# Kernel optimization log

Measured on AMD Instinct MI355X. Metric: run time of the kernel, lower is better.

Reference implementation:

```python
import jax, jax.numpy as jnp
import numpy as np

N = 20000; E = 320000; G = 64; IN = 64; HID = 128; H = 8; HD = H * HID  # 1024


def setup_inputs() -> dict:
    key = jax.random.key(0)
    ks = jax.random.split(key, 32)
    inp = {}
    inp['x'] = jax.random.normal(ks[0], (N, IN), jnp.float32)
    inp['edge_index'] = jax.random.randint(ks[1], (2, E), 0, N, dtype=jnp.int64)
    inp['batch'] = jnp.sort(jax.random.randint(ks[2], (N,), 0, G, dtype=jnp.int64))
    dims_in = [IN, HD, HD]
    k = 3
    for i in range(3):
        d_in = dims_in[i]
        inp[f'gat_W{i}'] = jax.random.normal(ks[k], (d_in, HD), jnp.float32) * (1.0 / np.sqrt(d_in)); k += 1
        inp[f'gat_b{i}'] = jnp.zeros((HD,), jnp.float32)
        inp[f'att_src{i}'] = jax.random.normal(ks[k], (H, HID), jnp.float32) * 0.1; k += 1
        inp[f'att_dst{i}'] = jax.random.normal(ks[k], (H, HID), jnp.float32) * 0.1; k += 1
    for i in range(2):
        inp[f'boot_W{i}'] = jax.random.normal(ks[k], (HD, HD), jnp.float32) * (1.0 / np.sqrt(HD)); k += 1
        inp[f'boot_b{i}'] = jnp.zeros((HD,), jnp.float32)
    inp['clf_W1'] = jax.random.normal(ks[k], (HD, HID), jnp.float32) * (1.0 / np.sqrt(HD)); k += 1
    inp['clf_b1'] = jnp.zeros((HID,), jnp.float32)
    inp['clf_W2'] = jax.random.normal(ks[k], (HID, 2), jnp.float32) * (1.0 / np.sqrt(HID)); k += 1
    inp['clf_b2'] = jnp.zeros((2,), jnp.float32)
    return inp


def _gat_layer(x, W, b, a_src, a_dst, src, dst):
    # PyG GATConv (concat=True, self-loops already appended, eval mode => no dropout)
    h = (x @ W).reshape(N, H, HID)                      # [N,H,D]
    s = jnp.einsum('nhd,hd->nh', h, a_src)              # [N,H]
    t = jnp.einsum('nhd,hd->nh', h, a_dst)              # [N,H]
    e = jax.nn.leaky_relu(s[src] + t[dst], 0.2)         # [Etot,H]
    m = jax.ops.segment_max(e, dst, num_segments=N)     # segment softmax over incoming edges
    m = jnp.where(jnp.isfinite(m), m, 0.0)
    ex = jnp.exp(e - m[dst])
    denom = jax.ops.segment_sum(ex, dst, num_segments=N)
    alpha = ex / jnp.maximum(denom[dst], 1e-16)         # [Etot,H]
    out = jax.ops.segment_sum(alpha[:, :, None] * h[src], dst, num_segments=N)  # [N,H,D]
    return out.reshape(N, HD) + b


def reference(x, edge_index, batch,
              gat_W0, gat_b0, att_src0, att_dst0,
              gat_W1, gat_b1, att_src1, att_dst1,
              gat_W2, gat_b2, att_src2, att_dst2,
              boot_W0, boot_b0, boot_W1, boot_b1,
              clf_W1, clf_b1, clf_W2, clf_b2):
    loop = jnp.arange(N, dtype=edge_index.dtype)
    src = jnp.concatenate([edge_index[0], loop])
    dst = jnp.concatenate([edge_index[1], loop])
    gat = [(gat_W0, gat_b0, att_src0, att_dst0),
           (gat_W1, gat_b1, att_src1, att_dst1),
           (gat_W2, gat_b2, att_src2, att_dst2)]
    boot = [(boot_W0, boot_b0), (boot_W1, boot_b1)]
    h = x
    for i in range(3):
        W, b, a_s, a_d = gat[i]
        h = jax.nn.elu(_gat_layer(h, W, b, a_s, a_d, src, dst))
        if i < 2:
            noise = jax.random.normal(jax.random.key(100 + i), h.shape, h.dtype) * 0.1
            bW, bb = boot[i]
            h = (h + noise) @ bW + bb
    # global mean pool over graphs
    sums = jax.ops.segment_sum(h, batch, num_segments=G)        # [G,HD]
    cnts = jax.ops.segment_sum(jnp.ones((N,), h.dtype), batch, num_segments=G)
    g = sums / jnp.maximum(cnts, 1.0)[:, None]
    z = jax.nn.relu(g @ clf_W1 + clf_b1)                        # dropout = identity (eval)
    return z @ clf_W2 + clf_b2
```

## Files before the change

### kernel.cpp

```cpp
#include <hip/hip_runtime.h>
#include <stdint.h>

#define N_NODES 20000
#define N_EDGES 320000
#define E_TOT   (N_EDGES + N_NODES)
#define NGRAPH  64
#define DIN     64
#define DHID    128
#define NHEAD   8
#define HDIM    1024

typedef unsigned int u32;
typedef unsigned short u16;
typedef __bf16 bfx8 __attribute__((ext_vector_type(8)));
typedef float f32x4 __attribute__((ext_vector_type(4)));
typedef float f32x2 __attribute__((ext_vector_type(2)));

__device__ __forceinline__ u16 f2bf(float f){
  u32 u = __float_as_uint(f);
  u32 r = (u + 0x7FFFu + ((u >> 16) & 1u)) >> 16;
  return (u16)r;
}
__device__ __forceinline__ float bf2f(u16 v){
  return __uint_as_float(((u32)v) << 16);
}
__device__ __forceinline__ f32x2 up2(u32 u){
  f32x2 v;
  v.x = __uint_as_float(u << 16);
  v.y = __uint_as_float(u & 0xffff0000u);
  return v;
}

typedef __attribute__((address_space(3))) u32 lds_u32_t;
typedef const __attribute__((address_space(1))) u32 glb_u32_t;
__device__ __forceinline__ void g2l16(const void* g, void* l){
  __builtin_amdgcn_global_load_lds((glb_u32_t*)(uintptr_t)g,
                                   (lds_u32_t*)(uintptr_t)l, 16, 0, 0);
}

__device__ __forceinline__ u32 rotl32(u32 x, int r){ return (x<<r) | (x>>(32-r)); }

__device__ __forceinline__ void threefry2x32(u32 k0, u32 k1, u32 x0, u32 x1,
                                             u32& y0, u32& y1){
  u32 k2 = k0 ^ k1 ^ 0x1BD11BDAu;
  x0 += k0; x1 += k1;
#define TFR(r) { x0 += x1; x1 = rotl32(x1, (r)); x1 ^= x0; }
  TFR(13) TFR(15) TFR(26) TFR(6)
  x0 += k1; x1 += k2 + 1u;
  TFR(17) TFR(29) TFR(16) TFR(24)
  x0 += k2; x1 += k0 + 2u;
  TFR(13) TFR(15) TFR(26) TFR(6)
  x0 += k0; x1 += k1 + 3u;
  TFR(17) TFR(29) TFR(16) TFR(24)
  x0 += k1; x1 += k2 + 4u;
  TFR(13) TFR(15) TFR(26) TFR(6)
  x0 += k2; x1 += k0 + 5u;
#undef TFR
  y0 = x0; y1 = x1;
}

__device__ __forceinline__ float erfinv_fast(float x){
  float t = fmaf(-x, x, 1.0f);
  float w = -__logf(t);
  float p;
  if (w < 5.0f){
    w -= 2.5f;
    p = 2.81022636e-08f;
    p = fmaf(p, w, 3.43273939e-07f);
    p = fmaf(p, w, -3.5233877e-06f);
    p = fmaf(p, w, -4.39150654e-06f);
    p = fmaf(p, w, 0.00021858087f);
    p = fmaf(p, w, -0.00125372503f);
    p = fmaf(p, w, -0.00417768164f);
    p = fmaf(p, w, 0.246640727f);
    p = fmaf(p, w, 1.50140941f);
  } else {
    w = sqrtf(w) - 3.0f;
    p = -0.000200214257f;
    p = fmaf(p, w, 0.000100950558f);
    p = fmaf(p, w, 0.00134934322f);
    p = fmaf(p, w, -0.00367342844f);
    p = fmaf(p, w, 0.00573950773f);
    p = fmaf(p, w, -0.0076224613f);
    p = fmaf(p, w, 0.00943887047f);
    p = fmaf(p, w, 1.00167406f);
    p = fmaf(p, w, 2.83297682f);
  }
  return p * x;
}

__device__ __forceinline__ float jax_normal(u32 seed, u32 i){
  u32 y0, y1;
  threefry2x32(0u, seed, 0u, i, y0, y1);
  u32 bits = y0 ^ y1;
  float f = __uint_as_float((bits >> 9) | 0x3f800000u) - 1.0f;
  float xx = fmaxf(-0.99999994f, fmaf(f, 2.0f, -0.99999994f));
  return 1.41421356f * erfinv_fast(xx);
}

__global__ __launch_bounds__(256) void prep_misc_kernel(const float* __restrict__ x,
    const float* __restrict__ W0, const float* __restrict__ W1,
    u16* __restrict__ xbf, u16* __restrict__ O0, u16* __restrict__ O1,
    const int* __restrict__ ei, const int* __restrict__ batch,
    int* __restrict__ cnt, int* __restrict__ gcnt,
    const float* __restrict__ gatW0, const float* __restrict__ asrc0,
    const float* __restrict__ adst0, float* __restrict__ wst){
  const int z = blockIdx.y;
  if (z < 3){
    const float* S = (z==0) ? W0 : (z==1) ? W1 : x;
    u16* D = (z==0) ? O0 : (z==1) ? O1 : xbf;
    const int total = (z==2) ? N_NODES*DIN : HDIM*HDIM;
    int i = (blockIdx.x*256 + threadIdx.x)*4;
    if (i < total){
      float4 v = *(const float4*)(S + i);
      D[i+0] = f2bf(v.x); D[i+1] = f2bf(v.y);
      D[i+2] = f2bf(v.z); D[i+3] = f2bf(v.w);
    }
  } else if (z == 3){
    int i = blockIdx.x*256 + threadIdx.x;
    if (i < N_EDGES) atomicAdd(&cnt[ei[N_EDGES + i]], 1);
    else if (i < E_TOT) atomicAdd(&gcnt[batch[i - N_EDGES]], 1);
  } else {
    if (blockIdx.x == 0){
      for (int o = threadIdx.x; o < DIN*16; o += 256){
        const int d = o >> 4, c = o & 15;
        const int hh = c & 7;
        const float* av = ((c < 8) ? asrc0 : adst0) + hh*DHID;
        const float* wr = gatW0 + (size_t)d*HDIM + hh*DHID;
        float a = 0.f;
        for (int k = 0; k < DHID; ++k) a = fmaf(wr[k], av[k], a);
        wst[o] = a;
      }
    }
  }
}

__global__ __launch_bounds__(256) void st0_kernel(const float* __restrict__ x,
    const float* __restrict__ wst, float* __restrict__ sbuf,
    float* __restrict__ tbuf){
  const int n = blockIdx.x*256 + threadIdx.x;
  if (n >= N_NODES) return;
  float acc[16];
#pragma unroll
  for (int c = 0; c < 16; ++c) acc[c] = 0.f;
  const float* xr = x + (size_t)n*DIN;
  for (int d = 0; d < DIN; d += 4){
    const float4 xv = *(const float4*)(xr + d);
    const float* w0 = wst + d*16;
#pragma unroll
    for (int c = 0; c < 16; ++c){
      acc[c] = fmaf(xv.x, w0[c],      acc[c]);
      acc[c] = fmaf(xv.y, w0[16+c],   acc[c]);
      acc[c] = fmaf(xv.z, w0[32+c],   acc[c]);
      acc[c] = fmaf(xv.w, w0[48+c],   acc[c]);
    }
  }
#pragma unroll
  for (int h = 0; h < NHEAD; ++h){
    sbuf[n*NHEAD + h] = acc[h];
    tbuf[n*NHEAD + h] = acc[8 + h];
  }
}

__global__ __launch_bounds__(256) void transpose_all_kernel(
    const float* __restrict__ W0, const float* __restrict__ W1,
    const float* __restrict__ W2,
    u16* __restrict__ T0, u16* __restrict__ T1, u16* __restrict__ T2){
  const int z = blockIdx.z;
  const float* W = (z==0)?W0:(z==1)?W1:W2;
  u16* T = (z==0)?T0:(z==1)?T1:T2;
  const int K = (z==0)?DIN:HDIM;
  const int bk = blockIdx.y*32;
  if (bk >= K) return;
  __shared__ float t[32][33];
  int bn = blockIdx.x*32;
  int lx = threadIdx.x & 31, ly = threadIdx.x >> 5;
#pragma unroll
  for (int r = 0; r < 32; r += 8)
    t[ly+r][lx] = W[(size_t)(bk+ly+r)*HDIM + bn + lx];
  __syncthreads();
#pragma unroll
  for (int r = 0; r < 32; r += 8){
    const u16 v = f2bf(t[lx][ly+r]);
    if (z == 0){
      const size_t base = (size_t)(bn+ly+r)*128 + bk + lx;
      T[base] = v; T[base + 64] = v;
    } else {
      T[(size_t)(bn+ly+r)*K + bk + lx] = v;
    }
  }
}

__global__ __launch_bounds__(1024) void scan_pair_kernel(const int* __restrict__ cnt,
    int* __restrict__ rowptr, int* __restrict__ cursor, int* __restrict__ colidx,
    const int* __restrict__ gcnt, int* __restrict__ goff){
  if (blockIdx.x == 1){
    if (threadIdx.x == 0){
      int s = 0;
      for (int g = 0; g < NGRAPH; ++g){ goff[g] = s; s += gcnt[g]; }
      goff[NGRAPH] = s;
    }
    return;
  }
  __shared__ int wsum[16];
  __shared__ int carry_s;
  const int tid = threadIdx.x, lane = tid & 63, wv = tid >> 6;
  if (tid == 0){ carry_s = 0; rowptr[0] = 0; }
  __syncthreads();
  for (int base = 0; base < N_NODES; base += 1024){
    int i = base + tid;
    int v = (i < N_NODES) ? cnt[i] + 1 : 0;
    int s = v;
#pragma unroll
    for (int off = 1; off < 64; off <<= 1){
      int t = __shfl_up(s, off);
      if (lane >= off) s += t;
    }
    if (lane == 63) wsum[wv] = s;
    __syncthreads();
    if (wv == 0 && lane < 16){
      int ws = wsum[lane];
#pragma unroll
      for (int off = 1; off < 16; off <<= 1){
        int t = __shfl_up(ws, off);
        if (lane >= off) ws += t;
      }
      wsum[lane] = ws;
    }
    __syncthreads();
    int incl = s + ((wv > 0) ? wsum[wv-1] : 0) + carry_s;
    if (i < N_NODES){
      rowptr[i+1] = incl;
      const int slot = incl - v;
      colidx[slot] = i;
      cursor[i] = slot + 1;
    }
    __syncthreads();
    if (tid == 1023) carry_s = incl;
    __syncthreads();
  }
}

__global__ __launch_bounds__(256) void fill_edges_kernel(const int* __restrict__ ei,
    int* __restrict__ cursor, int* __restrict__ colidx){
  int e = blockIdx.x*256 + threadIdx.x;
  if (e < N_EDGES){
    int s = ei[e], d = ei[N_EDGES + e];
    int p = atomicAdd(&cursor[d], 1);
    colidx[p] = s;
  }
}

__device__ __forceinline__ void gemm_tile(const u16* __restrict__ A,
    const u16* __restrict__ BT, const float* __restrict__ bias,
    u16* __restrict__ Cb, int M, int K, int bm, int bn,
    u16* As, u16* Bs,
    const float* __restrict__ asrc, const float* __restrict__ adst,
    float* __restrict__ sbuf, float* __restrict__ tbuf,
    const int emode, const u32 seed){
  const int tid = threadIdx.x;
  const int lane = tid & 63, w = tid >> 6;
  const int wm = (w & 1)*64, wn = (w >> 1)*64;

  const int cid0 = tid, cid1 = 256 + tid;
  const int r0 = cid0 & 127, kc0 = cid0 >> 7;
  const int r1 = cid1 & 127, kc1 = cid1 >> 7;
  int ar0 = bm + r0; if (ar0 >= M) ar0 = M - 1;
  int ar1 = bm + r1; if (ar1 >= M) ar1 = M - 1;
  const u16* ag0 = A + (size_t)ar0*K + kc0*8;
  const u16* ag1 = A + (size_t)ar1*K + kc1*8;
  const u16* bg0 = BT + (size_t)(bn + r0)*K + kc0*8;
  const u16* bg1 = BT + (size_t)(bn + r1)*K + kc1*8;
  u16* al0 = As + cid0*8;  u16* al1 = As + cid1*8;
  u16* bl0 = Bs + cid0*8;  u16* bl1 = Bs + cid1*8;

  const int rowl = lane & 15, kg = lane >> 4;
  const bfx8* ap = (const bfx8*)(As + ((size_t)kg*128 + wm + rowl)*8);
  const bfx8* bp = (const bfx8*)(Bs + ((size_t)kg*128 + wn + rowl)*8);

  f32x4 acc[4][4] = {};
  for (int k0 = 0; k0 < K; k0 += 32){
    g2l16(ag0 + k0, al0);
    g2l16(ag1 + k0, al1);
    g2l16(bg0 + k0, bl0);
    g2l16(bg1 + k0, bl1);
    __syncthreads();
    bfx8 af[4], bfr[4];
#pragma unroll
    for (int i = 0; i < 4; ++i){ af[i] = ap[i*16]; bfr[i] = bp[i*16]; }
#pragma unroll
    for (int i = 0; i < 4; ++i)
#pragma unroll
      for (int j = 0; j < 4; ++j)
        acc[j][i] = __builtin_amdgcn_mfma_f32_16x16x32_bf16(bfr[j], af[i], acc[j][i], 0, 0, 0);
    __syncthreads();
  }

  const int quad = lane >> 4;
  const bool dost = (sbuf != nullptr);
  const int head = bn >> 7;
  float sl[4] = {0.f,0.f,0.f,0.f}, tl[4] = {0.f,0.f,0.f,0.f};
#pragma unroll
  for (int j = 0; j < 4; ++j){
    const int col0 = bn + wn + j*16 + quad*4;
    float4 bv = make_float4(0.f,0.f,0.f,0.f);
    if (bias) bv = *(const float4*)(bias + col0);
    float4 av = make_float4(0.f,0.f,0.f,0.f), dv = av;
    if (dost){
      const int d0 = col0 - bn;
      av = *(const float4*)(asrc + head*DHID + d0);
      dv = *(const float4*)(adst + head*DHID + d0);
    }
#pragma unroll
    for (int i = 0; i < 4; ++i){
      const int row = bm + wm + i*16 + rowl;
      if (emode == 1){
        if (row < M){
          float v0 = acc[j][i][0] + bv.x;
          float v1 = acc[j][i][1] + bv.y;
          float v2 = acc[j][i][2] + bv.z;
          float v3 = acc[j][i][3] + bv.w;
          v0 = (v0 > 0.f) ? v0 : __expf(v0) - 1.0f;
          v1 = (v1 > 0.f) ? v1 : __expf(v1) - 1.0f;
          v2 = (v2 > 0.f) ? v2 : __expf(v2) - 1.0f;
          v3 = (v3 > 0.f) ? v3 : __expf(v3) - 1.0f;
          const u32 ib = (u32)row*HDIM + (u32)col0;
          v0 = fmaf(0.1f, jax_normal(seed, ib+0u), v0);
          v1 = fmaf(0.1f, jax_normal(seed, ib+1u), v1);
          v2 = fmaf(0.1f, jax_normal(seed, ib+2u), v2);
          v3 = fmaf(0.1f, jax_normal(seed, ib+3u), v3);
          uint2 pk;
          pk.x = (u32)f2bf(v0) | ((u32)f2bf(v1) << 16);
          pk.y = (u32)f2bf(v2) | ((u32)f2bf(v3) << 16);
          *(uint2*)(Cb + (size_t)row*HDIM + col0) = pk;
        }
      } else {
        const u16 p0 = f2bf(acc[j][i][0] + bv.x);
        const u16 p1 = f2bf(acc[j][i][1] + bv.y);
        const u16 p2 = f2bf(acc[j][i][2] + bv.z);
        const u16 p3 = f2bf(acc[j][i][3] + bv.w);
        if (row < M){
          uint2 pk;
          pk.x = (u32)p0 | ((u32)p1 << 16);
          pk.y = (u32)p2 | ((u32)p3 << 16);
          *(uint2*)(Cb + (size_t)row*HDIM + col0) = pk;
        }
        if (dost){
          const float c0 = bf2f(p0), c1 = bf2f(p1), c2 = bf2f(p2), c3 = bf2f(p3);
          sl[i] = fmaf(c0, av.x, fmaf(c1, av.y, fmaf(c2, av.z, fmaf(c3, av.w, sl[i]))));
          tl[i] = fmaf(c0, dv.x, fmaf(c1, dv.y, fmaf(c2, dv.z, fmaf(c3, dv.w, tl[i]))));
        }
      }
    }
  }
  if (dost){
#pragma unroll
    for (int i = 0; i < 4; ++i){
      sl[i] += __shfl_xor(sl[i], 16); sl[i] += __shfl_xor(sl[i], 32);
      tl[i] += __shfl_xor(tl[i], 16); tl[i] += __shfl_xor(tl[i], 32);
    }
    float* sred = (float*)As;
    float* tred = sred + 128;
    if ((w >> 1) == 0 && quad == 0){
#pragma unroll
      for (int i = 0; i < 4; ++i){
        const int rl = wm + i*16 + rowl;
        sred[rl] = sl[i]; tred[rl] = tl[i];
      }
    }
    __syncthreads();
    if ((w >> 1) == 1 && quad == 0){
#pragma unroll
      for (int i = 0; i < 4; ++i){
        const int rl = wm + i*16 + rowl;
        const int row = bm + rl;
        if (row < M){
          sbuf[row*NHEAD + head] = sred[rl] + sl[i];
          tbuf[row*NHEAD + head] = tred[rl] + tl[i];
        }
      }
    }
  }
}

__global__ __launch_bounds__(256) void gemm_bf16(
    const u16* __restrict__ A, const u16* __restrict__ BT,
    const float* __restrict__ bias, u16* __restrict__ Cb, int M, int K,
    const float* __restrict__ asrc, const float* __restrict__ adst,
    float* __restrict__ sbuf, float* __restrict__ tbuf){
  __shared__ __align__(16) u16 As[4*128*8];
  __shared__ __align__(16) u16 Bs[4*128*8];
  const int kblk = blockIdx.y*8 + blockIdx.x;
  const int xc = kblk & 7, bq = (kblk >> 3) & 7, gq = kblk >> 6;
  const int bmi = gq*8 + xc;
  const int mt = (M + 127) >> 7;
  if (bmi >= mt) return;
  gemm_tile(A, BT, bias, Cb, M, K, bmi*128, bq*128, As, Bs,
            asrc, adst, sbuf, tbuf, 0, 0u);
}

__global__ __launch_bounds__(256) void gemm_l0t(
    const u16* __restrict__ agg2, const u16* __restrict__ BT,
    const float* __restrict__ bias, u16* __restrict__ Cb, u32 seed){
  __shared__ __align__(16) u16 As[4*128*8];
  __shared__ __align__(16) u16 Bs[4*128*8];
  const int head = blockIdx.x;
  const int bm = blockIdx.y*128;
  gemm_tile(agg2 + (size_t)head*N_NODES*128, BT, bias, Cb, N_NODES, 128,
            bm, head*128, As, Bs, nullptr, nullptr, nullptr, nullptr,
            1, seed);
}

__global__ __launch_bounds__(256) void wf_bias_kernel(
    const u16* __restrict__ A0, const u16* __restrict__ B0, u16* __restrict__ C0,
    const u16* __restrict__ A1, const u16* __restrict__ B1, u16* __restrict__ C1,
    const float* __restrict__ bb0, const u16* __restrict__ gwt0,
    const float* __restrict__ bb1, const u16* __restrict__ gwt1,
    float* __restrict__ fb0, float* __restrict__ fb1){
  __shared__ __align__(16) u16 As[4*128*8];
  __shared__ __align__(16) u16 Bs[4*128*8];
  if (blockIdx.z < 2){
    const u16* A = blockIdx.z ? A1 : A0;
    const u16* B = blockIdx.z ? B1 : B0;
    u16* C = blockIdx.z ? C1 : C0;
    gemm_tile(A, B, nullptr, C, HDIM, HDIM, blockIdx.y*128, blockIdx.x*128,
              As, Bs, nullptr, nullptr, nullptr, nullptr, 0, 0u);
  } else {
    const int kb = blockIdx.y*8 + blockIdx.x;
    const int wv = threadIdx.x >> 6, lane = threadIdx.x & 63;
    for (int idx = kb*4 + wv; idx < 2*HDIM; idx += 256){
      const int set = idx >> 10, n = idx & (HDIM-1);
      const float* bb = set ? bb1 : bb0;
      const u16* row = (set ? gwt1 : gwt0) + (size_t)n*HDIM + lane*16;
      const float* bp = bb + lane*16;
      float acc = 0.f;
#pragma unroll
      for (int k = 0; k < 16; ++k) acc = fmaf(bp[k], bf2f(row[k]), acc);
      for (int off = 32; off > 0; off >>= 1) acc += __shfl_down(acc, off);
      if (lane == 0) (set ? fb1 : fb0)[n] = acc;
    }
  }
}

__device__ __forceinline__ void gat_core(const u16* __restrict__ hlin,
    const float* __restrict__ sbuf, const float* __restrict__ tbuf,
    const int* __restrict__ rowptr, const int* __restrict__ colidx,
    const float* __restrict__ bias, const int n, const int lane,
    float o[16]){
  const int jsub = lane >> 3;
  const int hh   = lane & 7;
  const int hA   = lane >> 3;
  const int row0 = rowptr[n];
  const int deg  = rowptr[n+1] - row0;
  const float tn = tbuf[n*NHEAD + hh];
  const char* hl = (const char*)hlin;
  const u32 lb   = (u32)lane << 5;

  f32x2 acc[8] = {};
  float m_run = -INFINITY, d_run = 0.f;

  for (int c = 0; c < deg; c += 8){
    const int ne = min(8, deg - c);
    const int jj = (jsub < ne) ? jsub : (ne - 1);
    const int srcv = colidx[row0 + c + jj];
    float e = sbuf[srcv*NHEAD + hh] + tn;
    e = (e > 0.f) ? e : 0.2f*e;
    if (jsub >= ne) e = -INFINITY;
    float mc = e;
    mc = fmaxf(mc, __shfl_xor(mc, 8));
    mc = fmaxf(mc, __shfl_xor(mc, 16));
    mc = fmaxf(mc, __shfl_xor(mc, 32));
    const float mnew = fmaxf(m_run, mc);
    const float w = __expf(e - mnew);
    float ws = w;
    ws += __shfl_xor(ws, 8);
    ws += __shfl_xor(ws, 16);
    ws += __shfl_xor(ws, 32);
    const float r = (m_run == -INFINITY) ? 0.0f : __expf(m_run - mnew);
    d_run = fmaf(d_run, r, ws);
    m_run = mnew;
    const float rA = __shfl(r, hA);
    const f32x2 r2 = {rA, rA};
#pragma unroll
    for (int q = 0; q < 8; ++q) acc[q] *= r2;
    int j = 0;
    for (; j + 2 <= ne; j += 2){
      const int s0 = __builtin_amdgcn_readlane(srcv, j*8);
      const int s1 = __builtin_amdgcn_readlane(srcv, j*8 + 8);
      const float w0 = __shfl(w, j*8 + hA);
      const float w1 = __shfl(w, j*8 + 8 + hA);
      const char* rp0 = hl + (((size_t)(u32)s0) << 11);
      const char* rp1 = hl + (((size_t)(u32)s1) << 11);
      const uint4 a0 = *(const uint4*)(rp0 + lb);
      const uint4 a1 = *(const uint4*)(rp0 + lb + 16);
      const uint4 b0 = *(const uint4*)(rp1 + lb);
      const uint4 b1 = *(const uint4*)(rp1 + lb + 16);
      const f32x2 w02 = {w0, w0}, w12 = {w1, w1};
      acc[0] = __builtin_elementwise_fma(w02, up2(a0.x), acc[0]);
      acc[1] = __builtin_elementwise_fma(w02, up2(a0.y), acc[1]);
      acc[2] = __builtin_elementwise_fma(w02, up2(a0.z), acc[2]);
      acc[3] = __builtin_elementwise_fma(w02, up2(a0.w), acc[3]);
      acc[4] = __builtin_elementwise_fma(w02, up2(a1.x), acc[4]);
      acc[5] = __builtin_elementwise_fma(w02, up2(a1.y), acc[5]);
      acc[6] = __builtin_elementwise_fma(w02, up2(a1.z), acc[6]);
      acc[7] = __builtin_elementwise_fma(w02, up2(a1.w), acc[7]);
      acc[0] = __builtin_elementwise_fma(w12, up2(b0.x), acc[0]);
      acc[1] = __builtin_elementwise_fma(w12, up2(b0.y), acc[1]);
      acc[2] = __builtin_elementwise_fma(w12, up2(b0.z), acc[2]);
      acc[3] = __builtin_elementwise_fma(w12, up2(b0.w), acc[3]);
      acc[4] = __builtin_elementwise_fma(w12, up2(b1.x), acc[4]);
      acc[5] = __builtin_elementwise_fma(w12, up2(b1.y), acc[5]);
      acc[6] = __builtin_elementwise_fma(w12, up2(b1.z), acc[6]);
      acc[7] = __builtin_elementwise_fma(w12, up2(b1.w), acc[7]);
    }
    if (j < ne){
      const int s0 = __builtin_amdgcn_readlane(srcv, j*8);
      const float w0 = __shfl(w, j*8 + hA);
      const char* rp0 = hl + (((size_t)(u32)s0) << 11);
      const uint4 a0 = *(const uint4*)(rp0 + lb);
      const uint4 a1 = *(const uint4*)(rp0 + lb + 16);
      const f32x2 w02 = {w0, w0};
      acc[0] = __builtin_elementwise_fma(w02, up2(a0.x), acc[0]);
      acc[1] = __builtin_elementwise_fma(w02, up2(a0.y), acc[1]);
      acc[2] = __builtin_elementwise_fma(w02, up2(a0.z), acc[2]);
      acc[3] = __builtin_elementwise_fma(w02, up2(a0.w), acc[3]);
      acc[4] = __builtin_elementwise_fma(w02, up2(a1.x), acc[4]);
      acc[5] = __builtin_elementwise_fma(w02, up2(a1.y), acc[5]);
      acc[6] = __builtin_elementwise_fma(w02, up2(a1.z), acc[6]);
      acc[7] = __builtin_elementwise_fma(w02, up2(a1.w), acc[7]);
    }
  }

  const float dA = __shfl(d_run, hA);
  const float invA = 1.0f / fmaxf(dA, 1e-16f);
#pragma unroll
  for (int q = 0; q < 8; ++q){ o[2*q] = acc[q].x; o[2*q+1] = acc[q].y; }
  const float4* bp = (const float4*)(bias + lane*16);
#pragma unroll
  for (int q = 0; q < 4; ++q){
    const float4 bv = bp[q];
    o[4*q+0] = fmaf(o[4*q+0], invA, bv.x);
    o[4*q+1] = fmaf(o[4*q+1], invA, bv.y);
    o[4*q+2] = fmaf(o[4*q+2], invA, bv.z);
    o[4*q+3] = fmaf(o[4*q+3], invA, bv.w);
  }
#pragma unroll
  for (int k = 0; k < 16; ++k)
    o[k] = (o[k] > 0.f) ? o[k] : __expf(o[k]) - 1.0f;
}

__global__ __launch_bounds__(256) void gat_agg_noise_kernel(
    const u16* __restrict__ hlin,
    const float* __restrict__ sbuf, const float* __restrict__ tbuf,
    const int* __restrict__ rowptr, const int* __restrict__ colidx,
    const float* __restrict__ bias, u16* __restrict__ outbf, u32 seed){
  const int tid  = threadIdx.x;
  const int lane = tid & 63;
  const int n    = blockIdx.x*4 + (tid >> 6);
  float o[16];
  gat_core(hlin, sbuf, tbuf, rowptr, colidx, bias, n, lane, o);
  const u32 ib = (u32)n*HDIM + (u32)lane*16u;
  u32 pk[8];
#pragma unroll
  for (int q = 0; q < 8; ++q){
    const float v0 = fmaf(0.1f, jax_normal(seed, ib + 2u*q + 0u), o[2*q+0]);
    const float v1 = fmaf(0.1f, jax_normal(seed, ib + 2u*q + 1u), o[2*q+1]);
    pk[q] = (u32)f2bf(v0) | ((u32)f2bf(v1) << 16);
  }
  uint4* dst = (uint4*)(outbf + (size_t)n*HDIM + lane*16);
  dst[0] = make_uint4(pk[0], pk[1], pk[2], pk[3]);
  dst[1] = make_uint4(pk[4], pk[5], pk[6], pk[7]);
}

__global__ __launch_bounds__(256) void gat_agg_pool_kernel(
    const u16* __restrict__ hlin,
    const float* __restrict__ sbuf, const float* __restrict__ tbuf,
    const int* __restrict__ rowptr, const int* __restrict__ colidx,
    const float* __restrict__ bias,
    const int* __restrict__ batch, float* __restrict__ gsum8){
  __shared__ float red[4][HDIM];
  const int tid  = threadIdx.x;
  const int lane = tid & 63;
  const int wv   = tid >> 6;
  const int n    = blockIdx.x*4 + wv;
  float o[16];
  gat_core(hlin, sbuf, tbuf, rowptr, colidx, bias, n, lane, o);
  float* rw = &red[wv][lane*16];
#pragma unroll
  for (int q = 0; q < 4; ++q)
    *(float4*)(rw + q*4) = make_float4(o[4*q], o[4*q+1], o[4*q+2], o[4*q+3]);
  __syncthreads();
  const int rep = blockIdx.x & 7;
  const int g0 = batch[blockIdx.x*4];
  const int g3 = batch[blockIdx.x*4 + 3];
  if (g0 == g3){
    const int d = tid*4;
    float4 s;
    s.x = red[0][d+0] + red[1][d+0] + red[2][d+0] + red[3][d+0];
    s.y = red[0][d+1] + red[1][d+1] + red[2][d+1] + red[3][d+1];
    s.z = red[0][d+2] + red[1][d+2] + red[2][d+2] + red[3][d+2];
    s.w = red[0][d+3] + red[1][d+3] + red[2][d+3] + red[3][d+3];
    float* gp = gsum8 + ((size_t)rep*NGRAPH + g0)*HDIM + d;
    atomicAdd(gp+0, s.x); atomicAdd(gp+1, s.y);
    atomicAdd(gp+2, s.z); atomicAdd(gp+3, s.w);
  } else {
    const int gn = batch[n];
    float* gp = gsum8 + ((size_t)rep*NGRAPH + gn)*HDIM + lane*16;
#pragma unroll
    for (int k = 0; k < 16; ++k) atomicAdd(gp + k, o[k]);
  }
}

__global__ __launch_bounds__(256) void agg_x_kernel(const u16* __restrict__ xbf,
    const float* __restrict__ sbuf, const float* __restrict__ tbuf,
    const int* __restrict__ rowptr, const int* __restrict__ colidx,
    u16* __restrict__ agg2){
  const int tid  = threadIdx.x;
  const int lane = tid & 63;
  const int n    = blockIdx.x*4 + (tid >> 6);
  const int jsub = lane >> 3;
  const int hh   = lane & 7;
  const int hA   = lane >> 3;
  const int row0 = rowptr[n];
  const int deg  = rowptr[n+1] - row0;
  const float tn = tbuf[n*NHEAD + hh];
  const char* xb = (const char*)xbf;
  const u32 lb   = (u32)(lane & 7) << 4;

  f32x2 acc[4] = {};
  float m_run = -INFINITY, d_run = 0.f;

  for (int c = 0; c < deg; c += 8){
    const int ne = min(8, deg - c);
    const int jj = (jsub < ne) ? jsub : (ne - 1);
    const int srcv = colidx[row0 + c + jj];
    float e = sbuf[srcv*NHEAD + hh] + tn;
    e = (e > 0.f) ? e : 0.2f*e;
    if (jsub >= ne) e = -INFINITY;
    float mc = e;
    mc = fmaxf(mc, __shfl_xor(mc, 8));
    mc = fmaxf(mc, __shfl_xor(mc, 16));
    mc = fmaxf(mc, __shfl_xor(mc, 32));
    const float mnew = fmaxf(m_run, mc);
    const float w = __expf(e - mnew);
    float ws = w;
    ws += __shfl_xor(ws, 8);
    ws += __shfl_xor(ws, 16);
    ws += __shfl_xor(ws, 32);
    const float r = (m_run == -INFINITY) ? 0.0f : __expf(m_run - mnew);
    d_run = fmaf(d_run, r, ws);
    m_run = mnew;
    const float rA = __shfl(r, hA);
    const f32x2 r2 = {rA, rA};
#pragma unroll
    for (int q = 0; q < 4; ++q) acc[q] *= r2;
    int j = 0;
    for (; j + 2 <= ne; j += 2){
      const int s0 = __builtin_amdgcn_readlane(srcv, j*8);
      const int s1 = __builtin_amdgcn_readlane(srcv, j*8 + 8);
      const float w0 = __shfl(w, j*8 + hA);
      const float w1 = __shfl(w, j*8 + 8 + hA);
      const uint4 a0 = *(const uint4*)(xb + (((size_t)(u32)s0) << 7) + lb);
      const uint4 b0 = *(const uint4*)(xb + (((size_t)(u32)s1) << 7) + lb);
      const f32x2 w02 = {w0, w0}, w12 = {w1, w1};
      acc[0] = __builtin_elementwise_fma(w02, up2(a0.x), acc[0]);
      acc[1] = __builtin_elementwise_fma(w02, up2(a0.y), acc[1]);
      acc[2] = __builtin_elementwise_fma(w02, up2(a0.z), acc[2]);
      acc[3] = __builtin_elementwise_fma(w02, up2(a0.w), acc[3]);
      acc[0] = __builtin_elementwise_fma(w12, up2(b0.x), acc[0]);
      acc[1] = __builtin_elementwise_fma(w12, up2(b0.y), acc[1]);
      acc[2] = __builtin_elementwise_fma(w12, up2(b0.z), acc[2]);
      acc[3] = __builtin_elementwise_fma(w12, up2(b0.w), acc[3]);
    }
    if (j < ne){
      const int s0 = __builtin_amdgcn_readlane(srcv, j*8);
      const float w0 = __shfl(w, j*8 + hA);
      const uint4 a0 = *(const uint4*)(xb + (((size_t)(u32)s0) << 7) + lb);
      const f32x2 w02 = {w0, w0};
      acc[0] = __builtin_elementwise_fma(w02, up2(a0.x), acc[0]);
      acc[1] = __builtin_elementwise_fma(w02, up2(a0.y), acc[1]);
      acc[2] = __builtin_elementwise_fma(w02, up2(a0.z), acc[2]);
      acc[3] = __builtin_elementwise_fma(w02, up2(a0.w), acc[3]);
    }
  }

  const float dA = __shfl(d_run, hA);
  const float invA = 1.0f / fmaxf(dA, 1e-16f);
  float v[8];
#pragma unroll
  for (int q = 0; q < 4; ++q){ v[2*q] = acc[q].x*invA; v[2*q+1] = acc[q].y*invA; }
  u32 hp[4], lp[4];
#pragma unroll
  for (int q = 0; q < 4; ++q){
    const u16 h0 = f2bf(v[2*q]),   h1 = f2bf(v[2*q+1]);
    const u16 l0 = f2bf(v[2*q]   - bf2f(h0));
    const u16 l1 = f2bf(v[2*q+1] - bf2f(h1));
    hp[q] = (u32)h0 | ((u32)h1 << 16);
    lp[q] = (u32)l0 | ((u32)l1 << 16);
  }
  u16* base = agg2 + ((size_t)hA*N_NODES + (size_t)n)*128 + (lane & 7)*8;
  *(uint4*)(base)      = make_uint4(hp[0], hp[1], hp[2], hp[3]);
  *(uint4*)(base + 64) = make_uint4(lp[0], lp[1], lp[2], lp[3]);
}

__global__ __launch_bounds__(256) void pool_clf_kernel(const float* __restrict__ gsum8,
    const int* __restrict__ gcnt,
    const float* __restrict__ W1, const float* __restrict__ b1,
    const float* __restrict__ W2, const float* __restrict__ b2,
    float* __restrict__ out){
  __shared__ float gs[HDIM];
  __shared__ float z[DHID];
  const int g = blockIdx.x, tid = threadIdx.x;
  const int cb = tid*4;
  const float invc = 1.0f / fmaxf((float)gcnt[g], 1.0f);
  float4 s = make_float4(0.f,0.f,0.f,0.f);
#pragma unroll
  for (int r = 0; r < 8; ++r){
    const float4 v = *(const float4*)(gsum8 + ((size_t)r*NGRAPH + g)*HDIM + cb);
    s.x += v.x; s.y += v.y; s.z += v.z; s.w += v.w;
  }
  gs[cb+0] = s.x*invc; gs[cb+1] = s.y*invc;
  gs[cb+2] = s.z*invc; gs[cb+3] = s.w*invc;
  __syncthreads();
  if (tid < DHID){
    float a = b1[tid];
    for (int k = 0; k < HDIM; ++k) a = fmaf(gs[k], W1[k*DHID + tid], a);
    z[tid] = fmaxf(a, 0.0f);
  }
  __syncthreads();
  if (tid < 2){
    float o = b2[tid];
    for (int k = 0; k < DHID; ++k) o = fmaf(z[k], W2[k*2 + tid], o);
    out[g*2 + tid] = o;
  }
}

extern "C" void kernel_launch(void* const* d_in, const int* in_sizes, int n_in,
                              void* d_out, int out_size, void* d_ws, size_t ws_size,
                              hipStream_t stream){
  const float* x      = (const float*)d_in[0];
  const int*   ei     = (const int*)d_in[1];
  const int*   batch  = (const int*)d_in[2];
  const float* gatW[3]  = {(const float*)d_in[3],  (const float*)d_in[7],  (const float*)d_in[11]};
  const float* gatB[3]  = {(const float*)d_in[4],  (const float*)d_in[8],  (const float*)d_in[12]};
  const float* asrc[3]  = {(const float*)d_in[5],  (const float*)d_in[9],  (const float*)d_in[13]};
  const float* adst[3]  = {(const float*)d_in[6],  (const float*)d_in[10], (const float*)d_in[14]};
  const float* bootW[2] = {(const float*)d_in[15], (const float*)d_in[17]};
  const float* bootB[2] = {(const float*)d_in[16], (const float*)d_in[18]};
  const float* clfW1 = (const float*)d_in[19];
  const float* clfb1 = (const float*)d_in[20];
  const float* clfW2 = (const float*)d_in[21];
  const float* clfb2 = (const float*)d_in[22];
  float* outp = (float*)d_out;

  float* fws  = (float*)d_ws;
  float* hB   = fws;
  float* sbuf = hB + (size_t)N_NODES*HDIM;
  float* tbuf = sbuf + (size_t)N_NODES*NHEAD;
  float* fbias0 = tbuf + (size_t)N_NODES*NHEAD;
  float* fbias1 = fbias0 + HDIM;
  u16* xbf    = (u16*)(fbias1 + HDIM);
  u16* hAbf   = xbf + (size_t)N_NODES*DIN;
  u16* hBbf   = hAbf + (size_t)N_NODES*HDIM;
  u16* wt[3];
  wt[0] = hBbf + (size_t)N_NODES*HDIM;
  wt[1] = wt[0] + (size_t)HDIM*128;
  wt[2] = wt[1] + (size_t)HDIM*HDIM;
  u16* wnt0   = wt[2] + (size_t)HDIM*HDIM;
  u16* wnt1   = wnt0 + (size_t)HDIM*HDIM;
  u16* wf0    = wnt1 + (size_t)HDIM*HDIM;
  u16* wf1    = wf0 + (size_t)HDIM*HDIM;
  int* rowptr = (int*)(wf1 + (size_t)HDIM*HDIM);
  int* cursor = rowptr + (N_NODES+1);
  int* colidx = cursor + N_NODES;
  int* gcnt   = colidx + E_TOT;
  int* cnt    = gcnt + NGRAPH;
  float* gsum8 = (float*)(cnt + N_NODES);
  int* goff   = (int*)(gsum8 + (size_t)8*NGRAPH*HDIM);
  float* wst  = (float*)(goff + NGRAPH + 1);

  u16* agg2 = hAbf;

  (void)hipMemsetAsync(gcnt, 0,
      (NGRAPH + N_NODES + (size_t)8*NGRAPH*HDIM)*sizeof(int), stream);

  const int nb_e = (N_EDGES + 255)/256;

  prep_misc_kernel<<<dim3((E_TOT + 255)/256, 5), 256, 0, stream>>>(
      x, bootW[0], bootW[1], xbf, wnt0, wnt1, ei, batch, cnt, gcnt,
      gatW[0], asrc[0], adst[0], wst);
  st0_kernel<<<(N_NODES + 255)/256, 256, 0, stream>>>(x, wst, sbuf, tbuf);
  transpose_all_kernel<<<dim3(HDIM/32, HDIM/32, 3), 256, 0, stream>>>(
      gatW[0], gatW[1], gatW[2], wt[0], wt[1], wt[2]);
  scan_pair_kernel<<<2, 1024, 0, stream>>>(cnt, rowptr, cursor, colidx, gcnt, goff);
  fill_edges_kernel<<<nb_e, 256, 0, stream>>>(ei, cursor, colidx);

  wf_bias_kernel<<<dim3(8, 8, 3), 256, 0, stream>>>(
      wt[1], wnt0, wf0, wt[2], wnt1, wf1,
      bootB[0], wt[1], bootB[1], wt[2], fbias0, fbias1);

  const int mt = (N_NODES + 127)/128;
  dim3 gemmGrid(8, (mt + 7)/8*8);

  agg_x_kernel<<<N_NODES/4, 256, 0, stream>>>(xbf, sbuf, tbuf, rowptr, colidx,
                                              agg2);
  gemm_l0t<<<dim3(8, mt), 256, 0, stream>>>(agg2, wt[0], gatB[0], hBbf, 100u);

  gemm_bf16<<<gemmGrid, 256, 0, stream>>>(hBbf, wf0, fbias0, hAbf, N_NODES, HDIM,
                                          asrc[1], adst[1], sbuf, tbuf);
  gat_agg_noise_kernel<<<N_NODES/4, 256, 0, stream>>>(hAbf, sbuf, tbuf, rowptr,
                                                      colidx, gatB[1], hBbf, 101u);
  gemm_bf16<<<gemmGrid, 256, 0, stream>>>(hBbf, wf1, fbias1, hAbf, N_NODES, HDIM,
                                          asrc[2], adst[2], sbuf, tbuf);
  gat_agg_pool_kernel<<<N_NODES/4, 256, 0, stream>>>(hAbf, sbuf, tbuf, rowptr,
                                                     colidx, gatB[2], batch, gsum8);

  pool_clf_kernel<<<NGRAPH, 256, 0, stream>>>(gsum8, gcnt,
                                              clfW1, clfb1, clfW2, clfb2, outp);
}
```

Baseline: 829.7 us.

## Unroll edge gather loop by three and replace pooling atomics with partial-sum reduction

The edge aggregation loops in gat_core and agg_x now process three neighbour rows per iteration instead of two, with two- and one-edge tails. This puts more independent gathers in flight per wave. The final-layer pooling no longer does float atomics into eight replicated per-graph buffers. Blocks whose four nodes share a graph write their partial sums to a per-block scratch array, and a new pool_reduce_kernel sums those per graph; atomics remain only for boundary blocks. This adds a kernel launch and extra scratch traffic, and the unroll raises register pressure.

```diff
diff --git a/kernel.cpp b/kernel.cpp
--- a/kernel.cpp
+++ b/kernel.cpp
@@ -442,6 +442,16 @@
   }
 }
 
+#define EDGE_FMA(WV, R0, R1)                                              \
+  acc[0] = __builtin_elementwise_fma(WV, up2(R0.x), acc[0]);              \
+  acc[1] = __builtin_elementwise_fma(WV, up2(R0.y), acc[1]);              \
+  acc[2] = __builtin_elementwise_fma(WV, up2(R0.z), acc[2]);              \
+  acc[3] = __builtin_elementwise_fma(WV, up2(R0.w), acc[3]);              \
+  acc[4] = __builtin_elementwise_fma(WV, up2(R1.x), acc[4]);              \
+  acc[5] = __builtin_elementwise_fma(WV, up2(R1.y), acc[5]);              \
+  acc[6] = __builtin_elementwise_fma(WV, up2(R1.z), acc[6]);              \
+  acc[7] = __builtin_elementwise_fma(WV, up2(R1.w), acc[7]);
+
 __device__ __forceinline__ void gat_core(const u16* __restrict__ hlin,
     const float* __restrict__ sbuf, const float* __restrict__ tbuf,
     const int* __restrict__ rowptr, const int* __restrict__ colidx,
@@ -484,7 +494,28 @@
 #pragma unroll
     for (int q = 0; q < 8; ++q) acc[q] *= r2;
     int j = 0;
-    for (; j + 2 <= ne; j += 2){
+    for (; j + 3 <= ne; j += 3){
+      const int s0 = __builtin_amdgcn_readlane(srcv, j*8);
+      const int s1 = __builtin_amdgcn_readlane(srcv, j*8 + 8);
+      const int s2 = __builtin_amdgcn_readlane(srcv, j*8 + 16);
+      const float w0 = __shfl(w, j*8 + hA);
+      const float w1 = __shfl(w, j*8 + 8 + hA);
+      const float w2 = __shfl(w, j*8 + 16 + hA);
+      const char* rp0 = hl + (((size_t)(u32)s0) << 11);
+      const char* rp1 = hl + (((size_t)(u32)s1) << 11);
+      const char* rp2 = hl + (((size_t)(u32)s2) << 11);
+      const uint4 a0 = *(const uint4*)(rp0 + lb);
+      const uint4 a1 = *(const uint4*)(rp0 + lb + 16);
+      const uint4 b0 = *(const uint4*)(rp1 + lb);
+      const uint4 b1 = *(const uint4*)(rp1 + lb + 16);
+      const uint4 e0 = *(const uint4*)(rp2 + lb);
+      const uint4 e1 = *(const uint4*)(rp2 + lb + 16);
+      const f32x2 w02 = {w0, w0}, w12 = {w1, w1}, w22 = {w2, w2};
+      EDGE_FMA(w02, a0, a1)
+      EDGE_FMA(w12, b0, b1)
+      EDGE_FMA(w22, e0, e1)
+    }
+    if (j + 2 <= ne){
       const int s0 = __builtin_amdgcn_readlane(srcv, j*8);
       const int s1 = __builtin_amdgcn_readlane(srcv, j*8 + 8);
       const float w0 = __shfl(w, j*8 + hA);
@@ -496,22 +527,9 @@
       const uint4 b0 = *(const uint4*)(rp1 + lb);
       const uint4 b1 = *(const uint4*)(rp1 + lb + 16);
       const f32x2 w02 = {w0, w0}, w12 = {w1, w1};
-      acc[0] = __builtin_elementwise_fma(w02, up2(a0.x), acc[0]);
-      acc[1] = __builtin_elementwise_fma(w02, up2(a0.y), acc[1]);
-      acc[2] = __builtin_elementwise_fma(w02, up2(a0.z), acc[2]);
-      acc[3] = __builtin_elementwise_fma(w02, up2(a0.w), acc[3]);
-      acc[4] = __builtin_elementwise_fma(w02, up2(a1.x), acc[4]);
-      acc[5] = __builtin_elementwise_fma(w02, up2(a1.y), acc[5]);
-      acc[6] = __builtin_elementwise_fma(w02, up2(a1.z), acc[6]);
-      acc[7] = __builtin_elementwise_fma(w02, up2(a1.w), acc[7]);
-      acc[0] = __builtin_elementwise_fma(w12, up2(b0.x), acc[0]);
-      acc[1] = __builtin_elementwise_fma(w12, up2(b0.y), acc[1]);
-      acc[2] = __builtin_elementwise_fma(w12, up2(b0.z), acc[2]);
-      acc[3] = __builtin_elementwise_fma(w12, up2(b0.w), acc[3]);
-      acc[4] = __builtin_elementwise_fma(w12, up2(b1.x), acc[4]);
-      acc[5] = __builtin_elementwise_fma(w12, up2(b1.y), acc[5]);
-      acc[6] = __builtin_elementwise_fma(w12, up2(b1.z), acc[6]);
-      acc[7] = __builtin_elementwise_fma(w12, up2(b1.w), acc[7]);
+      EDGE_FMA(w02, a0, a1)
+      EDGE_FMA(w12, b0, b1)
+      j += 2;
     }
     if (j < ne){
       const int s0 = __builtin_amdgcn_readlane(srcv, j*8);
@@ -520,14 +538,7 @@
       const uint4 a0 = *(const uint4*)(rp0 + lb);
       const uint4 a1 = *(const uint4*)(rp0 + lb + 16);
       const f32x2 w02 = {w0, w0};
-      acc[0] = __builtin_elementwise_fma(w02, up2(a0.x), acc[0]);
-      acc[1] = __builtin_elementwise_fma(w02, up2(a0.y), acc[1]);
-      acc[2] = __builtin_elementwise_fma(w02, up2(a0.z), acc[2]);
-      acc[3] = __builtin_elementwise_fma(w02, up2(a0.w), acc[3]);
-      acc[4] = __builtin_elementwise_fma(w02, up2(a1.x), acc[4]);
-      acc[5] = __builtin_elementwise_fma(w02, up2(a1.y), acc[5]);
-      acc[6] = __builtin_elementwise_fma(w02, up2(a1.z), acc[6]);
-      acc[7] = __builtin_elementwise_fma(w02, up2(a1.w), acc[7]);
+      EDGE_FMA(w02, a0, a1)
     }
   }
 
@@ -577,7 +588,8 @@
     const float* __restrict__ sbuf, const float* __restrict__ tbuf,
     const int* __restrict__ rowptr, const int* __restrict__ colidx,
     const float* __restrict__ bias,
-    const int* __restrict__ batch, float* __restrict__ gsum8){
+    const int* __restrict__ batch, float* __restrict__ gsum,
+    float* __restrict__ pblk){
   __shared__ float red[4][HDIM];
   const int tid  = threadIdx.x;
   const int lane = tid & 63;
@@ -585,31 +597,50 @@
   const int n    = blockIdx.x*4 + wv;
   float o[16];
   gat_core(hlin, sbuf, tbuf, rowptr, colidx, bias, n, lane, o);
-  float* rw = &red[wv][lane*16];
-#pragma unroll
-  for (int q = 0; q < 4; ++q)
-    *(float4*)(rw + q*4) = make_float4(o[4*q], o[4*q+1], o[4*q+2], o[4*q+3]);
-  __syncthreads();
-  const int rep = blockIdx.x & 7;
   const int g0 = batch[blockIdx.x*4];
   const int g3 = batch[blockIdx.x*4 + 3];
   if (g0 == g3){
+    float* rw = &red[wv][lane*16];
+#pragma unroll
+    for (int q = 0; q < 4; ++q)
+      *(float4*)(rw + q*4) = make_float4(o[4*q], o[4*q+1], o[4*q+2], o[4*q+3]);
+    __syncthreads();
     const int d = tid*4;
     float4 s;
     s.x = red[0][d+0] + red[1][d+0] + red[2][d+0] + red[3][d+0];
     s.y = red[0][d+1] + red[1][d+1] + red[2][d+1] + red[3][d+1];
     s.z = red[0][d+2] + red[1][d+2] + red[2][d+2] + red[3][d+2];
     s.w = red[0][d+3] + red[1][d+3] + red[2][d+3] + red[3][d+3];
-    float* gp = gsum8 + ((size_t)rep*NGRAPH + g0)*HDIM + d;
-    atomicAdd(gp+0, s.x); atomicAdd(gp+1, s.y);
-    atomicAdd(gp+2, s.z); atomicAdd(gp+3, s.w);
+    *(float4*)(pblk + (size_t)blockIdx.x*HDIM + d) = s;
   } else {
     const int gn = batch[n];
-    float* gp = gsum8 + ((size_t)rep*NGRAPH + gn)*HDIM + lane*16;
+    float* gp = gsum + (size_t)gn*HDIM + lane*16;
 #pragma unroll
     for (int k = 0; k < 16; ++k) atomicAdd(gp + k, o[k]);
   }
 }
+
+__global__ __launch_bounds__(256) void pool_reduce_kernel(
+    const float* __restrict__ pblk, const int* __restrict__ batch,
+    const int* __restrict__ goff, float* __restrict__ gsum){
+  const int g = blockIdx.x;
+  const int d = blockIdx.y*256 + threadIdx.x;
+  const int n0 = goff[g], n1 = goff[g+1];
+  if (n0 >= n1) return;
+  const int c0 = n0 >> 2, c1 = (n1 - 1) >> 2;
+  float s = 0.f;
+  for (int c = c0; c <= c1; ++c){
+    if (batch[c*4] == g && batch[c*4 + 3] == g)
+      s += pblk[(size_t)c*HDIM + d];
+  }
+  gsum[(size_t)g*HDIM + d] += s;
+}
+
+#define EDGE_FMA4(WV, R0)                                                 \
+  acc[0] = __builtin_elementwise_fma(WV, up2(R0.x), acc[0]);              \
+  acc[1] = __builtin_elementwise_fma(WV, up2(R0.y), acc[1]);              \
+  acc[2] = __builtin_elementwise_fma(WV, up2(R0.z), acc[2]);              \
+  acc[3] = __builtin_elementwise_fma(WV, up2(R0.w), acc[3]);
 
 __global__ __launch_bounds__(256) void agg_x_kernel(const u16* __restrict__ xbf,
     const float* __restrict__ sbuf, const float* __restrict__ tbuf,
@@ -655,7 +686,22 @@
 #pragma unroll
     for (int q = 0; q < 4; ++q) acc[q] *= r2;
     int j = 0;
-    for (; j + 2 <= ne; j += 2){
+    for (; j + 3 <= ne; j += 3){
+      const int s0 = __builtin_amdgcn_readlane(srcv, j*8);
+      const int s1 = __builtin_amdgcn_readlane(srcv, j*8 + 8);
+      const int s2 = __builtin_amdgcn_readlane(srcv, j*8 + 16);
+      const float w0 = __shfl(w, j*8 + hA);
+      const float w1 = __shfl(w, j*8 + 8 + hA);
+      const float w2 = __shfl(w, j*8 + 16 + hA);
+      const uint4 a0 = *(const uint4*)(xb + (((size_t)(u32)s0) << 7) + lb);
+      const uint4 b0 = *(const uint4*)(xb + (((size_t)(u32)s1) << 7) + lb);
+      const uint4 e0 = *(const uint4*)(xb + (((size_t)(u32)s2) << 7) + lb);
+      const f32x2 w02 = {w0, w0}, w12 = {w1, w1}, w22 = {w2, w2};
+      EDGE_FMA4(w02, a0)
+      EDGE_FMA4(w12, b0)
+      EDGE_FMA4(w22, e0)
+    }
+    if (j + 2 <= ne){
       const int s0 = __builtin_amdgcn_readlane(srcv, j*8);
       const int s1 = __builtin_amdgcn_readlane(srcv, j*8 + 8);
       const float w0 = __shfl(w, j*8 + hA);
@@ -663,24 +709,16 @@
       const uint4 a0 = *(const uint4*)(xb + (((size_t)(u32)s0) << 7) + lb);
       const uint4 b0 = *(const uint4*)(xb + (((size_t)(u32)s1) << 7) + lb);
       const f32x2 w02 = {w0, w0}, w12 = {w1, w1};
-      acc[0] = __builtin_elementwise_fma(w02, up2(a0.x), acc[0]);
-      acc[1] = __builtin_elementwise_fma(w02, up2(a0.y), acc[1]);
-      acc[2] = __builtin_elementwise_fma(w02, up2(a0.z), acc[2]);
-      acc[3] = __builtin_elementwise_fma(w02, up2(a0.w), acc[3]);
-      acc[0] = __builtin_elementwise_fma(w12, up2(b0.x), acc[0]);
-      acc[1] = __builtin_elementwise_fma(w12, up2(b0.y), acc[1]);
-      acc[2] = __builtin_elementwise_fma(w12, up2(b0.z), acc[2]);
-      acc[3] = __builtin_elementwise_fma(w12, up2(b0.w), acc[3]);
+      EDGE_FMA4(w02, a0)
+      EDGE_FMA4(w12, b0)
+      j += 2;
     }
     if (j < ne){
       const int s0 = __builtin_amdgcn_readlane(srcv, j*8);
       const float w0 = __shfl(w, j*8 + hA);
       const uint4 a0 = *(const uint4*)(xb + (((size_t)(u32)s0) << 7) + lb);
       const f32x2 w02 = {w0, w0};
-      acc[0] = __builtin_elementwise_fma(w02, up2(a0.x), acc[0]);
-      acc[1] = __builtin_elementwise_fma(w02, up2(a0.y), acc[1]);
-      acc[2] = __builtin_elementwise_fma(w02, up2(a0.z), acc[2]);
-      acc[3] = __builtin_elementwise_fma(w02, up2(a0.w), acc[3]);
+      EDGE_FMA4(w02, a0)
     }
   }
 
@@ -703,7 +741,7 @@
   *(uint4*)(base + 64) = make_uint4(lp[0], lp[1], lp[2], lp[3]);
 }
 
-__global__ __launch_bounds__(256) void pool_clf_kernel(const float* __restrict__ gsum8,
+__global__ __launch_bounds__(256) void pool_clf_kernel(const float* __restrict__ gsum,
     const int* __restrict__ gcnt,
     const float* __restrict__ W1, const float* __restrict__ b1,
     const float* __restrict__ W2, const float* __restrict__ b2,
@@ -713,12 +751,7 @@
   const int g = blockIdx.x, tid = threadIdx.x;
   const int cb = tid*4;
   const float invc = 1.0f / fmaxf((float)gcnt[g], 1.0f);
-  float4 s = make_float4(0.f,0.f,0.f,0.f);
-#pragma unroll
-  for (int r = 0; r < 8; ++r){
-    const float4 v = *(const float4*)(gsum8 + ((size_t)r*NGRAPH + g)*HDIM + cb);
-    s.x += v.x; s.y += v.y; s.z += v.z; s.w += v.w;
-  }
+  const float4 s = *(const float4*)(gsum + (size_t)g*HDIM + cb);
   gs[cb+0] = s.x*invc; gs[cb+1] = s.y*invc;
   gs[cb+2] = s.z*invc; gs[cb+3] = s.w*invc;
   __syncthreads();
@@ -775,14 +808,15 @@
   int* colidx = cursor + N_NODES;
   int* gcnt   = colidx + E_TOT;
   int* cnt    = gcnt + NGRAPH;
-  float* gsum8 = (float*)(cnt + N_NODES);
-  int* goff   = (int*)(gsum8 + (size_t)8*NGRAPH*HDIM);
+  float* gsum = (float*)(cnt + N_NODES);
+  int* goff   = (int*)(gsum + (size_t)NGRAPH*HDIM);
   float* wst  = (float*)(goff + NGRAPH + 1);
 
-  u16* agg2 = hAbf;
+  u16* agg2  = hAbf;
+  float* pblk = hB;
 
   (void)hipMemsetAsync(gcnt, 0,
-      (NGRAPH + N_NODES + (size_t)8*NGRAPH*HDIM)*sizeof(int), stream);
+      (NGRAPH + N_NODES + NGRAPH*HDIM)*sizeof(int), stream);
 
   const int nb_e = (N_EDGES + 255)/256;
 
@@ -813,8 +847,10 @@
   gemm_bf16<<<gemmGrid, 256, 0, stream>>>(hBbf, wf1, fbias1, hAbf, N_NODES, HDIM,
                                           asrc[2], adst[2], sbuf, tbuf);
   gat_agg_pool_kernel<<<N_NODES/4, 256, 0, stream>>>(hAbf, sbuf, tbuf, rowptr,
-                                                     colidx, gatB[2], batch, gsum8);
-
-  pool_clf_kernel<<<NGRAPH, 256, 0, stream>>>(gsum8, gcnt,
+                                                     colidx, gatB[2], batch,
+                                                     gsum, pblk);
+  pool_reduce_kernel<<<dim3(NGRAPH, 4), 256, 0, stream>>>(pblk, batch, goff, gsum);
+
+  pool_clf_kernel<<<NGRAPH, 256, 0, stream>>>(gsum, gcnt,
                                               clfW1, clfb1, clfW2, clfb2, outp);
 }
```

Result: slower. 867.4 us (+4.5%).
